# Optimization experiments

Measured on AMD Instinct MI355X. Metric: run time of the kernel, lower is better.

Reference implementation:

```python
import jax, jax.numpy as jnp
import numpy as np
from jax import lax
from jax.scipy.special import logsumexp

XY, Z, V, WS = 16, 8, 10000, 2
S = XY * XY * Z            # 2048 states
EMB, TOK, HID = 256, 100, 256
B, T, L = 8, 16, 12
EPS = 1e-5


def residual(x, w1, b1, w2, b2, g, beta):
    # ResidualLayer: relu(lin1) -> relu(lin2) -> LayerNorm(x2 + x1)
    x1 = jax.nn.relu(x @ w1.T + b1)
    x2 = jax.nn.relu(x1 @ w2.T + b2)
    h = x2 + x1
    mu = h.mean(-1, keepdims=True)
    var = ((h - mu) ** 2).mean(-1, keepdims=True)
    return (h - mu) * lax.rsqrt(var + EPS) * g + beta


def win_logmean(m, axis, ws):
    win = 2 * ws + 1
    pads = [(0, 0)] * m.ndim
    pads[axis] = (ws, ws)
    p = jnp.pad(m, pads, mode='edge')
    d = m.shape[axis]
    acc = lax.dynamic_slice_in_dim(p, 0, d, axis)
    for k in range(1, win):
        acc = jnp.logaddexp(acc, lax.dynamic_slice_in_dim(p, k, d, axis))
    return acc - jnp.log(jnp.float32(win))


def setup_inputs() -> dict:
    key = jax.random.key(0)
    it = iter(jax.random.split(key, 64))

    def rn(shape, scale=0.05):
        return jax.random.normal(next(it), shape, jnp.float32) * scale

    inp = {}
    inp['state_emb'] = jax.random.normal(next(it), (S, EMB), jnp.float32)
    inp['tok_emb'] = jax.random.normal(next(it), (V, TOK), jnp.float32)

    def res(pfx, din, dout):
        inp[pfx + '_w1'] = rn((dout, din))
        inp[pfx + '_b1'] = jnp.zeros((dout,), jnp.float32)
        inp[pfx + '_w2'] = rn((dout, dout))
        inp[pfx + '_b2'] = jnp.zeros((dout,), jnp.float32)
        inp[pfx + '_g'] = jnp.ones((dout,), jnp.float32)
        inp[pfx + '_beta'] = jnp.zeros((dout,), jnp.float32)

    res('start', EMB, HID)
    inp['start_wo'] = rn((1, HID))
    inp['start_bo'] = jnp.zeros((1,), jnp.float32)
    res('tin', EMB, HID)
    res('tout', EMB, HID)
    res('emit', EMB, TOK)
    inp['stories'] = jax.random.randint(next(it), (B, T, L), 0, V + 1)  # id V = pad
    inp['story_length'] = T
    return inp


def reference(state_emb, tok_emb,
              start_w1, start_b1, start_w2, start_b2, start_g, start_beta, start_wo, start_bo,
              tin_w1, tin_b1, tin_w2, tin_b2, tin_g, tin_beta,
              tout_w1, tout_b1, tout_w2, tout_b2, tout_g, tout_beta,
              emit_w1, emit_b1, emit_w2, emit_b2, emit_g, emit_beta,
              stories, story_length):
    # prior_log_p: [S]
    h0 = residual(state_emb, start_w1, start_b1, start_w2, start_b2, start_g, start_beta)
    priors = jax.nn.log_softmax((h0 @ start_wo.T + start_bo)[:, 0], axis=-1)

    # transition_log_p: sparse-neighbor masked [S,S] log-softmax
    h_in = residual(state_emb, tin_w1, tin_b1, tin_w2, tin_b2, tin_g, tin_beta)
    h_out = residual(state_emb, tout_w1, tout_b1, tout_w2, tout_b2, tout_g, tout_beta)
    trans = h_in @ h_out.T
    idx = jnp.arange(S)
    offs = jnp.array([0, 1, -1, XY, -XY, XY * XY, 2 * XY * XY])
    neigh = idx[:, None] + offs[None, :]                        # [S,7]
    allowed = (neigh[:, :, None] == idx[None, None, :]).any(1)  # allowed[j,i]
    trans = jax.nn.log_softmax(jnp.where(allowed, trans, -jnp.inf), axis=-1)

    # emission matrix with windowed log-mean pooling over x,y
    h_emit = residual(state_emb, emit_w1, emit_b1, emit_w2, emit_b2, emit_g, emit_beta)
    em = jax.nn.log_softmax(h_emit @ tok_emb.T, axis=1)         # [S,V]
    em = em.reshape(Z, XY, XY, V)
    em = win_logmean(em, 2, WS)   # dim -2
    em = win_logmean(em, 1, WS)   # dim -3
    em = em.reshape(S, V)
    em_pad = jnp.concatenate([em, jnp.zeros((S, 1), em.dtype)], axis=1)  # pad token
    emis = em_pad.T[stories].sum(2)                             # [B,T,S]

    # HMM forward recursion in log domain
    score0 = emis[:, 0] + priors[None, :]

    def step(score, em_t):
        new = em_t + logsumexp(trans[None, :, :] + score[:, None, :], axis=-1)
        return new, new

    _, rest = lax.scan(step, score0, jnp.moveaxis(emis[:, 1:story_length], 1, 0))
    return jnp.concatenate([score0[None], rest], axis=0)        # [T,B,S]
```

## Files before the change

kernel.cpp:

```cpp
#include <hip/hip_runtime.h>
#include <hip/hip_bf16.h>
#include <math.h>


typedef __bf16 bf16_t;
typedef __bf16 bf16x8 __attribute__((ext_vector_type(8)));
typedef float  floatx4 __attribute__((ext_vector_type(4)));
typedef short  short8  __attribute__((ext_vector_type(8)));

#define S_TOT 2048
#define NT_LSE 157
#define LSE_LD 160


struct CJob { const float* src; void* dst; int srows, scols, drows, dcols, tobf; };
struct CJobs { CJob j[12]; };

__global__ void conv_k(CJobs jobs) {
    CJob job = jobs.j[blockIdx.y];
    int total = job.drows * job.dcols;
    for (int idx = blockIdx.x * 256 + threadIdx.x; idx < total; idx += gridDim.x * 256) {
        int r = idx / job.dcols;
        int c = idx - r * job.dcols;
        float v = (r < job.srows && c < job.scols) ? job.src[(size_t)r * job.scols + c] : 0.f;
        if (job.tobf) ((bf16_t*)job.dst)[idx] = (bf16_t)v;
        else          ((float*)job.dst)[idx]  = v;
    }
}

struct GJob {
    const bf16_t* A; int lda;
    const bf16_t* Bt; int ldb;
    int N, K;
    float* C; int ldc;
    const float* bias;
    const float* addm; int ldadd;
    bf16_t* Cbf; int ldcb;
    float* Pmax; float* Psum;
};
struct GJobs { GJob j[4]; };

#define BM 64
#define BN 64
#define LDT 72

template<int EPI>
__global__ __launch_bounds__(256) void gemm_k(GJobs jobs) {
    GJob jb = jobs.j[blockIdx.z];
    const int m0 = blockIdx.x * BM;
    const int n0 = blockIdx.y * BN;
    if (n0 >= jb.N) return;

    __shared__ alignas(16) bf16_t As[BM * LDT];
    __shared__ alignas(16) bf16_t Bs[BN * LDT];
    const int tid  = threadIdx.x;
    const int lane = tid & 63, wave = tid >> 6;
    const int wm = (wave & 1) * 32, wn = (wave >> 1) * 32;
    const int sr = tid >> 2, scc = (tid & 3) * 16;
    const int qm = lane & 15, qk = (lane >> 4) * 8;

    floatx4 acc[2][2];
    floatx4 zf = {0.f, 0.f, 0.f, 0.f};
#pragma unroll
    for (int i = 0; i < 2; i++)
#pragma unroll
        for (int j = 0; j < 2; j++) acc[i][j] = zf;

    for (int k0 = 0; k0 < jb.K; k0 += 64) {
        const bf16_t* Ar = jb.A + (size_t)(m0 + sr) * jb.lda + k0 + scc;
        const bf16_t* Br = jb.Bt + (size_t)(n0 + sr) * jb.ldb + k0 + scc;
        *(short8*)&As[sr * LDT + scc]     = *(const short8*)&Ar[0];
        *(short8*)&As[sr * LDT + scc + 8] = *(const short8*)&Ar[8];
        *(short8*)&Bs[sr * LDT + scc]     = *(const short8*)&Br[0];
        *(short8*)&Bs[sr * LDT + scc + 8] = *(const short8*)&Br[8];
        __syncthreads();
#pragma unroll
        for (int kk = 0; kk < 2; kk++) {
            int qo = kk * 32 + qk;
            bf16x8 a[2], b[2];
            a[0] = *(const bf16x8*)&As[(wm + qm) * LDT + qo];
            a[1] = *(const bf16x8*)&As[(wm + 16 + qm) * LDT + qo];
            b[0] = *(const bf16x8*)&Bs[(wn + qm) * LDT + qo];
            b[1] = *(const bf16x8*)&Bs[(wn + 16 + qm) * LDT + qo];
#pragma unroll
            for (int mi = 0; mi < 2; mi++)
#pragma unroll
                for (int ni = 0; ni < 2; ni++)
                    acc[mi][ni] = __builtin_amdgcn_mfma_f32_16x16x32_bf16(a[mi], b[ni], acc[mi][ni], 0, 0, 0);
        }
        __syncthreads();
    }

    const int cl = lane & 15, rq = (lane >> 4) * 4;

    if constexpr (EPI == 3) {
        __shared__ float Cs[BM][BN + 1];
#pragma unroll
        for (int mi = 0; mi < 2; mi++)
#pragma unroll
            for (int ni = 0; ni < 2; ni++)
#pragma unroll
                for (int r = 0; r < 4; r++) {
                    int lm = wm + mi * 16 + rq + r;
                    int ln2 = wn + ni * 16 + cl;
                    Cs[lm][ln2] = (n0 + ln2 < jb.N) ? acc[mi][ni][r] : -INFINITY;
                }
        __syncthreads();
        int trow = tid >> 2, part = tid & 3;
        float m = -INFINITY;
#pragma unroll
        for (int c = 0; c < 16; c++) m = fmaxf(m, Cs[trow][part * 16 + c]);
        m = fmaxf(m, __shfl_xor(m, 1));
        m = fmaxf(m, __shfl_xor(m, 2));
        float ss = 0.f;
#pragma unroll
        for (int c = 0; c < 16; c++) ss += __expf(Cs[trow][part * 16 + c] - m);
        ss += __shfl_xor(ss, 1);
        ss += __shfl_xor(ss, 2);
        if (part == 0) {
            jb.Pmax[(size_t)(m0 + trow) * LSE_LD + blockIdx.y] = m;
            jb.Psum[(size_t)(m0 + trow) * LSE_LD + blockIdx.y] = ss;
        }
    } else {
#pragma unroll
        for (int mi = 0; mi < 2; mi++)
#pragma unroll
            for (int ni = 0; ni < 2; ni++)
#pragma unroll
                for (int r = 0; r < 4; r++) {
                    int gm = m0 + wm + mi * 16 + rq + r;
                    int gn = n0 + wn + ni * 16 + cl;
                    if (gn < jb.N) {
                        float v = acc[mi][ni][r];
                        if constexpr (EPI == 0) {
                            jb.C[(size_t)gm * jb.ldc + gn] = v;
                        } else if constexpr (EPI == 1) {
                            v = fmaxf(v + jb.bias[gn], 0.f);
                            jb.C[(size_t)gm * jb.ldc + gn] = v;
                            jb.Cbf[(size_t)gm * jb.ldcb + gn] = (bf16_t)v;
                        } else {
                            v = fmaxf(v + jb.bias[gn], 0.f) + jb.addm[(size_t)gm * jb.ldadd + gn];
                            jb.C[(size_t)gm * jb.ldc + gn] = v;
                        }
                    }
                }
    }
}

struct LJob {
    const float* h; int ld, dout;
    const float* g; const float* beta;
    float* of32; int ldo;
    bf16_t* obf; int ldob; int padN;
    const float* wo; const float* bo; float* praw;
};
struct LJobs { LJob j[4]; };

__global__ __launch_bounds__(256) void ln_k(LJobs jobs) {
    LJob jb = jobs.j[blockIdx.y];
    __shared__ float red[256];
    int row = blockIdx.x, t = threadIdx.x;
    float hv = (t < jb.dout) ? jb.h[(size_t)row * jb.ld + t] : 0.f;
    red[t] = hv;
    __syncthreads();
#pragma unroll
    for (int s = 128; s > 0; s >>= 1) { if (t < s) red[t] += red[t + s]; __syncthreads(); }
    float mu = red[0] / jb.dout;
    __syncthreads();
    float d = (t < jb.dout) ? (hv - mu) : 0.f;
    red[t] = d * d;
    __syncthreads();
#pragma unroll
    for (int s = 128; s > 0; s >>= 1) { if (t < s) red[t] += red[t + s]; __syncthreads(); }
    float var = red[0] / jb.dout;
    float rstd = rsqrtf(var + 1e-5f);
    float y = 0.f;
    if (t < jb.dout) {
        y = d * rstd * jb.g[t] + jb.beta[t];
        if (jb.of32) jb.of32[(size_t)row * jb.ldo + t] = y;
        if (jb.obf)  jb.obf[(size_t)row * jb.ldob + t] = (bf16_t)y;
    } else if (jb.obf && t < jb.padN) {
        jb.obf[(size_t)row * jb.ldob + t] = (bf16_t)0.f;
    }
    if (jb.wo) {
        __syncthreads();
        red[t] = (t < jb.dout) ? y * jb.wo[t] : 0.f;
        __syncthreads();
#pragma unroll
        for (int s = 128; s > 0; s >>= 1) { if (t < s) red[t] += red[t + s]; __syncthreads(); }
        if (t == 0) jb.praw[row] = red[0] + jb.bo[0];
    }
}

__global__ __launch_bounds__(256) void trans_k(const float* __restrict__ hin,
                                               const float* __restrict__ hout,
                                               float* __restrict__ tr,
                                               const float* __restrict__ praw,
                                               float* __restrict__ plse)
{
    __shared__ float red[256];
    if (blockIdx.x == 512) {
        int t = threadIdx.x;
        float v[8];
        float m = -INFINITY;
#pragma unroll
        for (int i = 0; i < 8; i++) { v[i] = praw[t * 8 + i]; m = fmaxf(m, v[i]); }
        red[t] = m;
        __syncthreads();
#pragma unroll
        for (int s = 128; s > 0; s >>= 1) { if (t < s) red[t] = fmaxf(red[t], red[t + s]); __syncthreads(); }
        float M = red[0];
        __syncthreads();
        float ss = 0.f;
#pragma unroll
        for (int i = 0; i < 8; i++) ss += __expf(v[i] - M);
        red[t] = ss;
        __syncthreads();
#pragma unroll
        for (int s = 128; s > 0; s >>= 1) { if (t < s) red[t] += red[t + s]; __syncthreads(); }
        if (t == 0) plse[0] = M + __logf(red[0]);
        return;
    }
    const int OFFS[7] = {0, 1, -1, 16, -16, 256, 512};
    int j = blockIdx.x * 4 + (threadIdx.x >> 6);
    int lane = threadIdx.x & 63;
    float4 a = ((const float4*)(hin + (size_t)j * 256))[lane];
    float d[7];
#pragma unroll
    for (int k = 0; k < 7; k++) {
        int i = j + OFFS[k];
        float pdot = 0.f;
        if ((unsigned)i < 2048u) {
            float4 b = ((const float4*)(hout + (size_t)i * 256))[lane];
            pdot = a.x * b.x + a.y * b.y + a.z * b.z + a.w * b.w;
        }
#pragma unroll
        for (int o = 32; o > 0; o >>= 1) pdot += __shfl_down(pdot, o);
        d[k] = pdot;
    }
    if (lane == 0) {
        float m = -INFINITY;
#pragma unroll
        for (int k = 0; k < 7; k++) { int i = j + OFFS[k]; if ((unsigned)i < 2048u) m = fmaxf(m, d[k]); }
        float ss = 0.f;
#pragma unroll
        for (int k = 0; k < 7; k++) { int i = j + OFFS[k]; if ((unsigned)i < 2048u) ss += __expf(d[k] - m); }
        float l = __logf(ss);
#pragma unroll
        for (int k = 0; k < 7; k++) {
            int i = j + OFFS[k];
            tr[(size_t)j * 8 + k] = ((unsigned)i < 2048u) ? (d[k] - m - l) : -INFINITY;
        }
        tr[(size_t)j * 8 + 7] = -INFINITY;
    }
}

__global__ __launch_bounds__(256) void lse_fin_k(const float* __restrict__ Pmax,
                                                 const float* __restrict__ Psum,
                                                 float* __restrict__ lse)
{
    int s = (blockIdx.x * 256 + threadIdx.x) >> 6;
    int lane = threadIdx.x & 63;
    const float* pm = Pmax + (size_t)s * LSE_LD;
    const float* ps = Psum + (size_t)s * LSE_LD;
    float pv[3], sv[3];
    float m = -INFINITY;
#pragma unroll
    for (int i = 0; i < 3; i++) {
        int nb = i * 64 + lane;
        bool ok = nb < NT_LSE;
        pv[i] = ok ? pm[nb] : -INFINITY;
        sv[i] = ok ? ps[nb] : 0.f;
        m = fmaxf(m, pv[i]);
    }
#pragma unroll
    for (int o = 1; o < 64; o <<= 1) m = fmaxf(m, __shfl_xor(m, o));
    float ss = 0.f;
#pragma unroll
    for (int i = 0; i < 3; i++) ss += sv[i] * __expf(pv[i] - m);
#pragma unroll
    for (int o = 1; o < 64; o <<= 1) ss += __shfl_xor(ss, o);
    if (lane == 0) lse[s] = m + __logf(ss);
}

#define ELDT 136
__global__ __launch_bounds__(256) void empool_k(
    const float* __restrict__ tok_emb, const int* __restrict__ stories,
    const bf16_t* __restrict__ hemit, const float* __restrict__ lse,
    float* __restrict__ emis)
{
    __shared__ alignas(16) bf16_t As[16 * ELDT];
    __shared__ float Cs[16][260];
    __shared__ float sm2[256];
    __shared__ int stok[12];
    const int bt = blockIdx.x, z = blockIdx.y, t = threadIdx.x;
    if (t < 12) stok[t] = stories[bt * 12 + t];
    __syncthreads();
    {
        int row = t >> 4, c0 = (t & 15) * 8;
        int tok = (row < 12) ? stok[row] : 10000;
        const float* src = tok_emb + (size_t)tok * 100;
#pragma unroll
        for (int c = 0; c < 8; c++) {
            int cc = c0 + c;
            float v = (tok < 10000 && cc < 100) ? src[cc] : 0.f;
            As[row * ELDT + cc] = (bf16_t)v;
        }
    }
    __syncthreads();

    const int lane = t & 63, wave = t >> 6;
    const int qm = lane & 15, q = lane >> 4;
    floatx4 acc[4];
    floatx4 zf = {0.f, 0.f, 0.f, 0.f};
#pragma unroll
    for (int j = 0; j < 4; j++) acc[j] = zf;

#pragma unroll
    for (int kk = 0; kk < 4; kk++) {
        bf16x8 a = *(const bf16x8*)&As[qm * ELDT + kk * 32 + q * 8];
#pragma unroll
        for (int j = 0; j < 4; j++) {
            int nrow = z * 256 + (wave * 4 + j) * 16 + qm;
            bf16x8 b = *(const bf16x8*)&hemit[(size_t)nrow * 128 + kk * 32 + q * 8];
            acc[j] = __builtin_amdgcn_mfma_f32_16x16x32_bf16(a, b, acc[j], 0, 0, 0);
        }
    }
    {
        const int cl = lane & 15, rq = (lane >> 4) * 4;
#pragma unroll
        for (int j = 0; j < 4; j++) {
            int n = (wave * 4 + j) * 16 + cl;
            float ls = lse[z * 256 + n];
#pragma unroll
            for (int r = 0; r < 4; r++)
                Cs[rq + r][n] = acc[j][r] - ls;
        }
    }
    __syncthreads();

    const int a = t >> 4, b = t & 15;
    float accum = 0.f;
    for (int l = 0; l < 12; l++) {
        float m = -INFINITY;
#pragma unroll
        for (int d = -2; d <= 2; d++) {
            int bb = b + d; bb = bb < 0 ? 0 : (bb > 15 ? 15 : bb);
            m = fmaxf(m, Cs[l][a * 16 + bb]);
        }
        float ss = 0.f;
#pragma unroll
        for (int d = -2; d <= 2; d++) {
            int bb = b + d; bb = bb < 0 ? 0 : (bb > 15 ? 15 : bb);
            ss += __expf(Cs[l][a * 16 + bb] - m);
        }
        sm2[t] = m + __logf(ss);
        __syncthreads();
        float m2 = -INFINITY;
#pragma unroll
        for (int d = -2; d <= 2; d++) {
            int aa = a + d; aa = aa < 0 ? 0 : (aa > 15 ? 15 : aa);
            m2 = fmaxf(m2, sm2[aa * 16 + b]);
        }
        float s2 = 0.f;
#pragma unroll
        for (int d = -2; d <= 2; d++) {
            int aa = a + d; aa = aa < 0 ? 0 : (aa > 15 ? 15 : aa);
            s2 += __expf(sm2[aa * 16 + b] - m2);
        }
        if (stok[l] < 10000) accum += m2 + __logf(s2) - 3.2188758248682006f;
        __syncthreads();
    }
    emis[(size_t)bt * S_TOT + (size_t)z * 256 + t] = accum;
}

__global__ __launch_bounds__(1024) void fwd_k(const float* __restrict__ emm,
                                              const float* __restrict__ praw,
                                              const float* __restrict__ plse,
                                              const float* __restrict__ tr,
                                              float* __restrict__ out)
{
    const int OFFS[7] = {0, 1, -1, 16, -16, 256, 512};
    __shared__ float sc[2][S_TOT];
    int b = blockIdx.x, t = threadIdx.x;
    float pl = plse[0];
    const float* eb = emm + (size_t)b * 16 * S_TOT;

    float e[2][16];
#pragma unroll
    for (int i = 0; i < 2; i++) {
        int j = i * 1024 + t;
#pragma unroll
        for (int tt = 0; tt < 16; tt++) e[i][tt] = eb[tt * S_TOT + j];
    }
    float trj[2][7];
#pragma unroll
    for (int i = 0; i < 2; i++) {
        int j = i * 1024 + t;
        float4 lo = ((const float4*)(tr + (size_t)j * 8))[0];
        float4 hi = ((const float4*)(tr + (size_t)j * 8))[1];
        trj[i][0] = lo.x; trj[i][1] = lo.y; trj[i][2] = lo.z; trj[i][3] = lo.w;
        trj[i][4] = hi.x; trj[i][5] = hi.y; trj[i][6] = hi.z;
    }
#pragma unroll
    for (int i = 0; i < 2; i++) {
        int j = i * 1024 + t;
        float v = e[i][0] + praw[j] - pl;
        sc[0][j] = v;
        out[(size_t)b * S_TOT + j] = v;
    }
    __syncthreads();
#pragma unroll
    for (int tt = 1; tt < 16; tt++) {
        int cur = tt & 1, prv = cur ^ 1;
#pragma unroll
        for (int i = 0; i < 2; i++) {
            int j = i * 1024 + t;
            float x[7];
            float m = -INFINITY;
#pragma unroll
            for (int k = 0; k < 7; k++) {
                int ii = j + OFFS[k];
                ii = ii < 0 ? 0 : (ii > 2047 ? 2047 : ii);
                x[k] = trj[i][k] + sc[prv][ii];
                m = fmaxf(m, x[k]);
            }
            float ss = 0.f;
#pragma unroll
            for (int k = 0; k < 7; k++) ss += __expf(x[k] - m);
            float v = e[i][tt] + m + __logf(ss);
            sc[cur][j] = v;
            out[(size_t)tt * (8 * S_TOT) + (size_t)b * S_TOT + j] = v;
        }
        __syncthreads();
    }
}

extern "C" void kernel_launch(void* const* d_in, const int* in_sizes, int n_in,
                              void* d_out, int out_size, void* d_ws, size_t ws_size,
                              hipStream_t stream)
{
    (void)in_sizes; (void)n_in; (void)out_size; (void)ws_size;
    const float* state_emb  = (const float*)d_in[0];
    const float* tok_emb    = (const float*)d_in[1];
    const float* start_w1   = (const float*)d_in[2];
    const float* start_b1   = (const float*)d_in[3];
    const float* start_w2   = (const float*)d_in[4];
    const float* start_b2   = (const float*)d_in[5];
    const float* start_g    = (const float*)d_in[6];
    const float* start_beta = (const float*)d_in[7];
    const float* start_wo   = (const float*)d_in[8];
    const float* start_bo   = (const float*)d_in[9];
    const float* tin_w1     = (const float*)d_in[10];
    const float* tin_b1     = (const float*)d_in[11];
    const float* tin_w2     = (const float*)d_in[12];
    const float* tin_b2     = (const float*)d_in[13];
    const float* tin_g      = (const float*)d_in[14];
    const float* tin_beta   = (const float*)d_in[15];
    const float* tout_w1    = (const float*)d_in[16];
    const float* tout_b1    = (const float*)d_in[17];
    const float* tout_w2    = (const float*)d_in[18];
    const float* tout_b2    = (const float*)d_in[19];
    const float* tout_g     = (const float*)d_in[20];
    const float* tout_beta  = (const float*)d_in[21];
    const float* emit_w1    = (const float*)d_in[22];
    const float* emit_b1    = (const float*)d_in[23];
    const float* emit_w2    = (const float*)d_in[24];
    const float* emit_b2    = (const float*)d_in[25];
    const float* emit_g     = (const float*)d_in[26];
    const float* emit_beta  = (const float*)d_in[27];
    const int*   stories    = (const int*)d_in[28];
    float* out = (float*)d_out;

    char* base = (char*)d_ws;
    size_t off = 0;
    auto carve = [&](size_t bytes) -> char* {
        char* r = base + off;
        off = (off + bytes + 255) & ~(size_t)255;
        return r;
    };

    bf16_t* se_bf   = (bf16_t*)carve((size_t)2048 * 256 * 2);
    bf16_t* tok_bf  = (bf16_t*)carve((size_t)10048 * 128 * 2);
    bf16_t* w_s1    = (bf16_t*)carve((size_t)256 * 256 * 2);
    bf16_t* w_s2    = (bf16_t*)carve((size_t)256 * 256 * 2);
    bf16_t* w_i1    = (bf16_t*)carve((size_t)256 * 256 * 2);
    bf16_t* w_i2    = (bf16_t*)carve((size_t)256 * 256 * 2);
    bf16_t* w_o1    = (bf16_t*)carve((size_t)256 * 256 * 2);
    bf16_t* w_o2    = (bf16_t*)carve((size_t)256 * 256 * 2);
    bf16_t* w_e1    = (bf16_t*)carve((size_t)128 * 256 * 2);
    bf16_t* w_e2    = (bf16_t*)carve((size_t)128 * 128 * 2);
    float*  eb1     = (float*)carve(128 * 4);
    float*  eb2     = (float*)carve(128 * 4);
    bf16_t* hemit   = (bf16_t*)carve((size_t)2048 * 128 * 2);
    float*  hin     = (float*)carve((size_t)2048 * 256 * 4);
    float*  hout    = (float*)carve((size_t)2048 * 256 * 4);
    float*  praw    = (float*)carve((size_t)2048 * 4);
    float*  plse    = (float*)carve(256);
    float*  trans   = (float*)carve((size_t)2048 * 8 * 4);
    float*  pmax    = (float*)carve((size_t)2048 * LSE_LD * 4);
    float*  psum    = (float*)carve((size_t)2048 * LSE_LD * 4);
    float*  lse     = (float*)carve((size_t)2048 * 4);
    float*  emis    = (float*)carve((size_t)128 * 2048 * 4);

    size_t ovl = off;
    auto carveA = [&](size_t bytes) -> char* {
        char* r = base + ovl;
        ovl = (ovl + bytes + 255) & ~(size_t)255;
        return r;
    };
    float*  x1f_s  = (float*)carveA((size_t)2048 * 256 * 4);
    float*  x1f_i  = (float*)carveA((size_t)2048 * 256 * 4);
    float*  x1f_o  = (float*)carveA((size_t)2048 * 256 * 4);
    float*  x1f_e  = (float*)carveA((size_t)2048 * 128 * 4);
    bf16_t* x1b_s  = (bf16_t*)carveA((size_t)2048 * 256 * 2);
    bf16_t* x1b_i  = (bf16_t*)carveA((size_t)2048 * 256 * 2);
    bf16_t* x1b_o  = (bf16_t*)carveA((size_t)2048 * 256 * 2);
    bf16_t* x1b_e  = (bf16_t*)carveA((size_t)2048 * 128 * 2);
    float*  htmp_s = (float*)carveA((size_t)2048 * 256 * 4);
    float*  htmp_i = (float*)carveA((size_t)2048 * 256 * 4);
    float*  htmp_o = (float*)carveA((size_t)2048 * 256 * 4);
    float*  htmp_e = (float*)carveA((size_t)2048 * 128 * 4);

    CJobs cj;
    cj.j[0]  = {state_emb, se_bf, 2048, 256, 2048, 256, 1};
    cj.j[1]  = {tok_emb,   tok_bf, 10000, 100, 10048, 128, 1};
    cj.j[2]  = {start_w1,  w_s1, 256, 256, 256, 256, 1};
    cj.j[3]  = {start_w2,  w_s2, 256, 256, 256, 256, 1};
    cj.j[4]  = {tin_w1,    w_i1, 256, 256, 256, 256, 1};
    cj.j[5]  = {tin_w2,    w_i2, 256, 256, 256, 256, 1};
    cj.j[6]  = {tout_w1,   w_o1, 256, 256, 256, 256, 1};
    cj.j[7]  = {tout_w2,   w_o2, 256, 256, 256, 256, 1};
    cj.j[8]  = {emit_w1,   w_e1, 100, 256, 128, 256, 1};
    cj.j[9]  = {emit_w2,   w_e2, 100, 100, 128, 128, 1};
    cj.j[10] = {emit_b1,   eb1, 1, 100, 1, 128, 0};
    cj.j[11] = {emit_b2,   eb2, 1, 100, 1, 128, 0};
    conv_k<<<dim3(160, 12), 256, 0, stream>>>(cj);

    GJobs g1;
    g1.j[0] = {se_bf, 256, w_s1, 256, 256, 256, x1f_s, 256, start_b1, nullptr, 0, x1b_s, 256, nullptr, nullptr};
    g1.j[1] = {se_bf, 256, w_i1, 256, 256, 256, x1f_i, 256, tin_b1,   nullptr, 0, x1b_i, 256, nullptr, nullptr};
    g1.j[2] = {se_bf, 256, w_o1, 256, 256, 256, x1f_o, 256, tout_b1,  nullptr, 0, x1b_o, 256, nullptr, nullptr};
    g1.j[3] = {se_bf, 256, w_e1, 256, 128, 256, x1f_e, 128, eb1,      nullptr, 0, x1b_e, 128, nullptr, nullptr};
    gemm_k<1><<<dim3(32, 4, 4), 256, 0, stream>>>(g1);

    GJobs g2;
    g2.j[0] = {x1b_s, 256, w_s2, 256, 256, 256, htmp_s, 256, start_b2, x1f_s, 256, nullptr, 0, nullptr, nullptr};
    g2.j[1] = {x1b_i, 256, w_i2, 256, 256, 256, htmp_i, 256, tin_b2,   x1f_i, 256, nullptr, 0, nullptr, nullptr};
    g2.j[2] = {x1b_o, 256, w_o2, 256, 256, 256, htmp_o, 256, tout_b2,  x1f_o, 256, nullptr, 0, nullptr, nullptr};
    g2.j[3] = {x1b_e, 128, w_e2, 128, 128, 128, htmp_e, 128, eb2,      x1f_e, 128, nullptr, 0, nullptr, nullptr};
    gemm_k<2><<<dim3(32, 4, 4), 256, 0, stream>>>(g2);

    LJobs lj;
    lj.j[0] = {htmp_s, 256, 256, start_g, start_beta, nullptr, 0, nullptr, 0, 0, start_wo, start_bo, praw};
    lj.j[1] = {htmp_i, 256, 256, tin_g,   tin_beta,   hin, 256, nullptr, 0, 0, nullptr, nullptr, nullptr};
    lj.j[2] = {htmp_o, 256, 256, tout_g,  tout_beta,  hout, 256, nullptr, 0, 0, nullptr, nullptr, nullptr};
    lj.j[3] = {htmp_e, 128, 100, emit_g,  emit_beta,  nullptr, 0, hemit, 128, 128, nullptr, nullptr, nullptr};
    ln_k<<<dim3(2048, 4), 256, 0, stream>>>(lj);

    trans_k<<<513, 256, 0, stream>>>(hin, hout, trans, praw, plse);

    GJobs g3;
    g3.j[0] = {hemit, 128, tok_bf, 128, 10000, 128, nullptr, 0, nullptr, nullptr, 0, nullptr, 0, pmax, psum};
    gemm_k<3><<<dim3(32, NT_LSE, 1), 256, 0, stream>>>(g3);
    lse_fin_k<<<512, 256, 0, stream>>>(pmax, psum, lse);

    empool_k<<<dim3(128, 8), 256, 0, stream>>>(tok_emb, stories, hemit, lse, emis);

    fwd_k<<<8, 1024, 0, stream>>>(emis, praw, plse, trans, out);
}
```

Before: 221.8 us.

## Fuse fp32-to-bf16 conversion into GEMM loads and enlarge the vocab LSE GEMM tile

Drops the separate conversion kernel: the GEMMs now read fp32 weights, embeddings and tok_emb directly and convert to bf16 while staging into shared memory, with K and row padding handled by predicates. The vocab logsumexp GEMM becomes a dedicated kernel with 128x128 tiles and 4x4 MFMA per wave. It reduces partial max and sum within the block, halving the partial count that lse_fin_k combines. This removes one launch and the bf16 staging buffers' traffic, at the cost of extra conversion work in every GEMM tile load and higher register pressure in the larger tile.

```diff
diff --git a/kernel.cpp b/kernel.cpp
--- a/kernel.cpp
+++ b/kernel.cpp
@@ -9,34 +9,19 @@
 typedef short  short8  __attribute__((ext_vector_type(8)));
 
 #define S_TOT 2048
-#define NT_LSE 157
-#define LSE_LD 160
-
-
-struct CJob { const float* src; void* dst; int srows, scols, drows, dcols, tobf; };
-struct CJobs { CJob j[12]; };
-
-__global__ void conv_k(CJobs jobs) {
-    CJob job = jobs.j[blockIdx.y];
-    int total = job.drows * job.dcols;
-    for (int idx = blockIdx.x * 256 + threadIdx.x; idx < total; idx += gridDim.x * 256) {
-        int r = idx / job.dcols;
-        int c = idx - r * job.dcols;
-        float v = (r < job.srows && c < job.scols) ? job.src[(size_t)r * job.scols + c] : 0.f;
-        if (job.tobf) ((bf16_t*)job.dst)[idx] = (bf16_t)v;
-        else          ((float*)job.dst)[idx]  = v;
-    }
-}
+#define NT2 79
+#define LSE_LD 80
 
 struct GJob {
-    const bf16_t* A; int lda;
-    const bf16_t* Bt; int ldb;
-    int N, K;
+    const float*  Af;
+    const bf16_t* Ab;
+    int lda;
+    const float* B; int ldb;
+    int N, Nrows, K, Kvalid;
     float* C; int ldc;
-    const float* bias;
+    const float* bias; int nbias;
     const float* addm; int ldadd;
     bf16_t* Cbf; int ldcb;
-    float* Pmax; float* Psum;
 };
 struct GJobs { GJob j[4]; };
 
@@ -44,7 +29,7 @@
 #define BN 64
 #define LDT 72
 
-template<int EPI>
+template<int EPI, int A32>
 __global__ __launch_bounds__(256) void gemm_k(GJobs jobs) {
     GJob jb = jobs.j[blockIdx.z];
     const int m0 = blockIdx.x * BM;
@@ -66,13 +51,39 @@
 #pragma unroll
         for (int j = 0; j < 2; j++) acc[i][j] = zf;
 
+    const bool brv = (n0 + sr) < jb.Nrows;
+
     for (int k0 = 0; k0 < jb.K; k0 += 64) {
-        const bf16_t* Ar = jb.A + (size_t)(m0 + sr) * jb.lda + k0 + scc;
-        const bf16_t* Br = jb.Bt + (size_t)(n0 + sr) * jb.ldb + k0 + scc;
-        *(short8*)&As[sr * LDT + scc]     = *(const short8*)&Ar[0];
-        *(short8*)&As[sr * LDT + scc + 8] = *(const short8*)&Ar[8];
-        *(short8*)&Bs[sr * LDT + scc]     = *(const short8*)&Br[0];
-        *(short8*)&Bs[sr * LDT + scc + 8] = *(const short8*)&Br[8];
+        if constexpr (A32) {
+            const float* Ar = jb.Af + (size_t)(m0 + sr) * jb.lda + k0 + scc;
+            alignas(16) bf16_t ta[16];
+#pragma unroll
+            for (int i = 0; i < 4; i++) {
+                float4 f = ((const float4*)Ar)[i];
+                ta[i * 4 + 0] = (bf16_t)f.x; ta[i * 4 + 1] = (bf16_t)f.y;
+                ta[i * 4 + 2] = (bf16_t)f.z; ta[i * 4 + 3] = (bf16_t)f.w;
+            }
+            *(short8*)&As[sr * LDT + scc]     = *(short8*)&ta[0];
+            *(short8*)&As[sr * LDT + scc + 8] = *(short8*)&ta[8];
+        } else {
+            const bf16_t* Ar = jb.Ab + (size_t)(m0 + sr) * jb.lda + k0 + scc;
+            *(short8*)&As[sr * LDT + scc]     = *(const short8*)&Ar[0];
+            *(short8*)&As[sr * LDT + scc + 8] = *(const short8*)&Ar[8];
+        }
+        {
+            const float* Br = jb.B + (size_t)(n0 + sr) * jb.ldb + k0 + scc;
+            alignas(16) bf16_t tb[16];
+#pragma unroll
+            for (int i = 0; i < 4; i++) {
+                int c4 = k0 + scc + i * 4;
+                float4 f = {0.f, 0.f, 0.f, 0.f};
+                if (brv && c4 < jb.Kvalid) f = *(const float4*)&Br[i * 4];
+                tb[i * 4 + 0] = (bf16_t)f.x; tb[i * 4 + 1] = (bf16_t)f.y;
+                tb[i * 4 + 2] = (bf16_t)f.z; tb[i * 4 + 3] = (bf16_t)f.w;
+            }
+            *(short8*)&Bs[sr * LDT + scc]     = *(short8*)&tb[0];
+            *(short8*)&Bs[sr * LDT + scc + 8] = *(short8*)&tb[8];
+        }
         __syncthreads();
 #pragma unroll
         for (int kk = 0; kk < 2; kk++) {
@@ -92,59 +103,25 @@
     }
 
     const int cl = lane & 15, rq = (lane >> 4) * 4;
-
-    if constexpr (EPI == 3) {
-        __shared__ float Cs[BM][BN + 1];
-#pragma unroll
-        for (int mi = 0; mi < 2; mi++)
-#pragma unroll
-            for (int ni = 0; ni < 2; ni++)
-#pragma unroll
-                for (int r = 0; r < 4; r++) {
-                    int lm = wm + mi * 16 + rq + r;
-                    int ln2 = wn + ni * 16 + cl;
-                    Cs[lm][ln2] = (n0 + ln2 < jb.N) ? acc[mi][ni][r] : -INFINITY;
-                }
-        __syncthreads();
-        int trow = tid >> 2, part = tid & 3;
-        float m = -INFINITY;
-#pragma unroll
-        for (int c = 0; c < 16; c++) m = fmaxf(m, Cs[trow][part * 16 + c]);
-        m = fmaxf(m, __shfl_xor(m, 1));
-        m = fmaxf(m, __shfl_xor(m, 2));
-        float ss = 0.f;
-#pragma unroll
-        for (int c = 0; c < 16; c++) ss += __expf(Cs[trow][part * 16 + c] - m);
-        ss += __shfl_xor(ss, 1);
-        ss += __shfl_xor(ss, 2);
-        if (part == 0) {
-            jb.Pmax[(size_t)(m0 + trow) * LSE_LD + blockIdx.y] = m;
-            jb.Psum[(size_t)(m0 + trow) * LSE_LD + blockIdx.y] = ss;
-        }
-    } else {
-#pragma unroll
-        for (int mi = 0; mi < 2; mi++)
-#pragma unroll
-            for (int ni = 0; ni < 2; ni++)
-#pragma unroll
-                for (int r = 0; r < 4; r++) {
-                    int gm = m0 + wm + mi * 16 + rq + r;
-                    int gn = n0 + wn + ni * 16 + cl;
-                    if (gn < jb.N) {
-                        float v = acc[mi][ni][r];
-                        if constexpr (EPI == 0) {
-                            jb.C[(size_t)gm * jb.ldc + gn] = v;
-                        } else if constexpr (EPI == 1) {
-                            v = fmaxf(v + jb.bias[gn], 0.f);
-                            jb.C[(size_t)gm * jb.ldc + gn] = v;
-                            jb.Cbf[(size_t)gm * jb.ldcb + gn] = (bf16_t)v;
-                        } else {
-                            v = fmaxf(v + jb.bias[gn], 0.f) + jb.addm[(size_t)gm * jb.ldadd + gn];
-                            jb.C[(size_t)gm * jb.ldc + gn] = v;
-                        }
+#pragma unroll
+    for (int mi = 0; mi < 2; mi++)
+#pragma unroll
+        for (int ni = 0; ni < 2; ni++)
+#pragma unroll
+            for (int r = 0; r < 4; r++) {
+                int gm = m0 + wm + mi * 16 + rq + r;
+                int gn = n0 + wn + ni * 16 + cl;
+                if (gn < jb.N) {
+                    float bv = (gn < jb.nbias) ? jb.bias[gn] : 0.f;
+                    float v = fmaxf(acc[mi][ni][r] + bv, 0.f);
+                    if constexpr (EPI == 1) {
+                        jb.C[(size_t)gm * jb.ldc + gn] = v;
+                        jb.Cbf[(size_t)gm * jb.ldcb + gn] = (bf16_t)v;
+                    } else {
+                        jb.C[(size_t)gm * jb.ldc + gn] = v + jb.addm[(size_t)gm * jb.ldadd + gn];
                     }
                 }
-    }
+            }
 }
 
 struct LJob {
@@ -255,6 +232,114 @@
     }
 }
 
+#define LDT2 72
+__global__ __launch_bounds__(256) void lse_gemm_k(
+    const bf16_t* __restrict__ hemit, const float* __restrict__ tok_emb,
+    float* __restrict__ Pmax, float* __restrict__ Psum)
+{
+    __shared__ alignas(16) bf16_t As[128 * LDT2];
+    __shared__ alignas(16) bf16_t Bs[128 * LDT2];
+    __shared__ float pmS[2][128];
+    __shared__ float psS[2][128];
+    const int mb = blockIdx.x * 128;
+    const int n0 = blockIdx.y * 128;
+    const int tid  = threadIdx.x;
+    const int lane = tid & 63, wave = tid >> 6;
+    const int wm = (wave & 1) * 64, wn = (wave >> 1) * 64;
+    const int sr2 = tid >> 1, scc2 = (tid & 1) * 32;
+    const int qm = lane & 15, qk = (lane >> 4) * 8;
+
+    floatx4 acc[4][4];
+    floatx4 zf = {0.f, 0.f, 0.f, 0.f};
+#pragma unroll
+    for (int i = 0; i < 4; i++)
+#pragma unroll
+        for (int j = 0; j < 4; j++) acc[i][j] = zf;
+
+    const bool brv = (n0 + sr2) < 10000;
+    const float* Brow = tok_emb + (size_t)(n0 + sr2) * 100;
+    const bf16_t* Arow = hemit + (size_t)(mb + sr2) * 128;
+
+#pragma unroll
+    for (int k0 = 0; k0 < 128; k0 += 64) {
+#pragma unroll
+        for (int i = 0; i < 4; i++)
+            *(short8*)&As[sr2 * LDT2 + scc2 + i * 8] = *(const short8*)&Arow[k0 + scc2 + i * 8];
+        {
+            alignas(16) bf16_t tb[32];
+#pragma unroll
+            for (int i = 0; i < 8; i++) {
+                int c4 = k0 + scc2 + i * 4;
+                float4 f = {0.f, 0.f, 0.f, 0.f};
+                if (brv && c4 < 100) f = *(const float4*)&Brow[c4];
+                tb[i * 4 + 0] = (bf16_t)f.x; tb[i * 4 + 1] = (bf16_t)f.y;
+                tb[i * 4 + 2] = (bf16_t)f.z; tb[i * 4 + 3] = (bf16_t)f.w;
+            }
+#pragma unroll
+            for (int i = 0; i < 4; i++)
+                *(short8*)&Bs[sr2 * LDT2 + scc2 + i * 8] = *(short8*)&tb[i * 8];
+        }
+        __syncthreads();
+#pragma unroll
+        for (int kk = 0; kk < 2; kk++) {
+            int qo = kk * 32 + qk;
+            bf16x8 a[4], b[4];
+#pragma unroll
+            for (int mi = 0; mi < 4; mi++) a[mi] = *(const bf16x8*)&As[(wm + mi * 16 + qm) * LDT2 + qo];
+#pragma unroll
+            for (int ni = 0; ni < 4; ni++) b[ni] = *(const bf16x8*)&Bs[(wn + ni * 16 + qm) * LDT2 + qo];
+#pragma unroll
+            for (int mi = 0; mi < 4; mi++)
+#pragma unroll
+                for (int ni = 0; ni < 4; ni++)
+                    acc[mi][ni] = __builtin_amdgcn_mfma_f32_16x16x32_bf16(a[mi], b[ni], acc[mi][ni], 0, 0, 0);
+        }
+        __syncthreads();
+    }
+
+    const int cl = lane & 15, rq = (lane >> 4) * 4;
+    const int half = wn >> 6;
+#pragma unroll
+    for (int mi = 0; mi < 4; mi++) {
+#pragma unroll
+        for (int r = 0; r < 4; r++) {
+            float mm = -INFINITY;
+#pragma unroll
+            for (int ni = 0; ni < 4; ni++) {
+                int gcol = n0 + wn + ni * 16 + cl;
+                if (gcol < 10000) mm = fmaxf(mm, acc[mi][ni][r]);
+            }
+            mm = fmaxf(mm, __shfl_xor(mm, 1));
+            mm = fmaxf(mm, __shfl_xor(mm, 2));
+            mm = fmaxf(mm, __shfl_xor(mm, 4));
+            mm = fmaxf(mm, __shfl_xor(mm, 8));
+            float ss = 0.f;
+#pragma unroll
+            for (int ni = 0; ni < 4; ni++) {
+                int gcol = n0 + wn + ni * 16 + cl;
+                if (gcol < 10000) ss += __expf(acc[mi][ni][r] - mm);
+            }
+            ss += __shfl_xor(ss, 1);
+            ss += __shfl_xor(ss, 2);
+            ss += __shfl_xor(ss, 4);
+            ss += __shfl_xor(ss, 8);
+            if (cl == 0) {
+                int row = wm + mi * 16 + rq + r;
+                pmS[half][row] = mm;
+                psS[half][row] = ss;
+            }
+        }
+    }
+    __syncthreads();
+    if (tid < 128) {
+        float ma = pmS[0][tid], mb2 = pmS[1][tid];
+        float M = fmaxf(ma, mb2);
+        float S = psS[0][tid] * __expf(ma - M) + psS[1][tid] * __expf(mb2 - M);
+        Pmax[(size_t)(mb + tid) * LSE_LD + blockIdx.y] = M;
+        Psum[(size_t)(mb + tid) * LSE_LD + blockIdx.y] = S;
+    }
+}
+
 __global__ __launch_bounds__(256) void lse_fin_k(const float* __restrict__ Pmax,
                                                  const float* __restrict__ Psum,
                                                  float* __restrict__ lse)
@@ -263,12 +348,12 @@
     int lane = threadIdx.x & 63;
     const float* pm = Pmax + (size_t)s * LSE_LD;
     const float* ps = Psum + (size_t)s * LSE_LD;
-    float pv[3], sv[3];
+    float pv[2], sv[2];
     float m = -INFINITY;
 #pragma unroll
-    for (int i = 0; i < 3; i++) {
+    for (int i = 0; i < 2; i++) {
         int nb = i * 64 + lane;
-        bool ok = nb < NT_LSE;
+        bool ok = nb < NT2;
         pv[i] = ok ? pm[nb] : -INFINITY;
         sv[i] = ok ? ps[nb] : 0.f;
         m = fmaxf(m, pv[i]);
@@ -277,7 +362,7 @@
     for (int o = 1; o < 64; o <<= 1) m = fmaxf(m, __shfl_xor(m, o));
     float ss = 0.f;
 #pragma unroll
-    for (int i = 0; i < 3; i++) ss += sv[i] * __expf(pv[i] - m);
+    for (int i = 0; i < 2; i++) if (sv[i] > 0.f) ss += sv[i] * __expf(pv[i] - m);
 #pragma unroll
     for (int o = 1; o < 64; o <<= 1) ss += __shfl_xor(ss, o);
     if (lane == 0) lse[s] = m + __logf(ss);
@@ -480,76 +565,43 @@
         return r;
     };
 
-    bf16_t* se_bf   = (bf16_t*)carve((size_t)2048 * 256 * 2);
-    bf16_t* tok_bf  = (bf16_t*)carve((size_t)10048 * 128 * 2);
-    bf16_t* w_s1    = (bf16_t*)carve((size_t)256 * 256 * 2);
-    bf16_t* w_s2    = (bf16_t*)carve((size_t)256 * 256 * 2);
-    bf16_t* w_i1    = (bf16_t*)carve((size_t)256 * 256 * 2);
-    bf16_t* w_i2    = (bf16_t*)carve((size_t)256 * 256 * 2);
-    bf16_t* w_o1    = (bf16_t*)carve((size_t)256 * 256 * 2);
-    bf16_t* w_o2    = (bf16_t*)carve((size_t)256 * 256 * 2);
-    bf16_t* w_e1    = (bf16_t*)carve((size_t)128 * 256 * 2);
-    bf16_t* w_e2    = (bf16_t*)carve((size_t)128 * 128 * 2);
-    float*  eb1     = (float*)carve(128 * 4);
-    float*  eb2     = (float*)carve(128 * 4);
-    bf16_t* hemit   = (bf16_t*)carve((size_t)2048 * 128 * 2);
-    float*  hin     = (float*)carve((size_t)2048 * 256 * 4);
-    float*  hout    = (float*)carve((size_t)2048 * 256 * 4);
-    float*  praw    = (float*)carve((size_t)2048 * 4);
-    float*  plse    = (float*)carve(256);
-    float*  trans   = (float*)carve((size_t)2048 * 8 * 4);
-    float*  pmax    = (float*)carve((size_t)2048 * LSE_LD * 4);
-    float*  psum    = (float*)carve((size_t)2048 * LSE_LD * 4);
-    float*  lse     = (float*)carve((size_t)2048 * 4);
-    float*  emis    = (float*)carve((size_t)128 * 2048 * 4);
-
-    size_t ovl = off;
-    auto carveA = [&](size_t bytes) -> char* {
-        char* r = base + ovl;
-        ovl = (ovl + bytes + 255) & ~(size_t)255;
-        return r;
-    };
-    float*  x1f_s  = (float*)carveA((size_t)2048 * 256 * 4);
-    float*  x1f_i  = (float*)carveA((size_t)2048 * 256 * 4);
-    float*  x1f_o  = (float*)carveA((size_t)2048 * 256 * 4);
-    float*  x1f_e  = (float*)carveA((size_t)2048 * 128 * 4);
-    bf16_t* x1b_s  = (bf16_t*)carveA((size_t)2048 * 256 * 2);
-    bf16_t* x1b_i  = (bf16_t*)carveA((size_t)2048 * 256 * 2);
-    bf16_t* x1b_o  = (bf16_t*)carveA((size_t)2048 * 256 * 2);
-    bf16_t* x1b_e  = (bf16_t*)carveA((size_t)2048 * 128 * 2);
-    float*  htmp_s = (float*)carveA((size_t)2048 * 256 * 4);
-    float*  htmp_i = (float*)carveA((size_t)2048 * 256 * 4);
-    float*  htmp_o = (float*)carveA((size_t)2048 * 256 * 4);
-    float*  htmp_e = (float*)carveA((size_t)2048 * 128 * 4);
-
-    CJobs cj;
-    cj.j[0]  = {state_emb, se_bf, 2048, 256, 2048, 256, 1};
-    cj.j[1]  = {tok_emb,   tok_bf, 10000, 100, 10048, 128, 1};
-    cj.j[2]  = {start_w1,  w_s1, 256, 256, 256, 256, 1};
-    cj.j[3]  = {start_w2,  w_s2, 256, 256, 256, 256, 1};
-    cj.j[4]  = {tin_w1,    w_i1, 256, 256, 256, 256, 1};
-    cj.j[5]  = {tin_w2,    w_i2, 256, 256, 256, 256, 1};
-    cj.j[6]  = {tout_w1,   w_o1, 256, 256, 256, 256, 1};
-    cj.j[7]  = {tout_w2,   w_o2, 256, 256, 256, 256, 1};
-    cj.j[8]  = {emit_w1,   w_e1, 100, 256, 128, 256, 1};
-    cj.j[9]  = {emit_w2,   w_e2, 100, 100, 128, 128, 1};
-    cj.j[10] = {emit_b1,   eb1, 1, 100, 1, 128, 0};
-    cj.j[11] = {emit_b2,   eb2, 1, 100, 1, 128, 0};
-    conv_k<<<dim3(160, 12), 256, 0, stream>>>(cj);
+    bf16_t* hemit = (bf16_t*)carve((size_t)2048 * 128 * 2);
+    float*  hin   = (float*)carve((size_t)2048 * 256 * 4);
+    float*  hout  = (float*)carve((size_t)2048 * 256 * 4);
+    float*  praw  = (float*)carve((size_t)2048 * 4);
+    float*  plse  = (float*)carve(256);
+    float*  trans = (float*)carve((size_t)2048 * 8 * 4);
+    float*  pmax  = (float*)carve((size_t)2048 * LSE_LD * 4);
+    float*  psum  = (float*)carve((size_t)2048 * LSE_LD * 4);
+    float*  lse   = (float*)carve((size_t)2048 * 4);
+    float*  emis  = (float*)carve((size_t)128 * 2048 * 4);
+
+    float*  x1f_s  = (float*)carve((size_t)2048 * 256 * 4);
+    float*  x1f_i  = (float*)carve((size_t)2048 * 256 * 4);
+    float*  x1f_o  = (float*)carve((size_t)2048 * 256 * 4);
+    float*  x1f_e  = (float*)carve((size_t)2048 * 128 * 4);
+    bf16_t* x1b_s  = (bf16_t*)carve((size_t)2048 * 256 * 2);
+    bf16_t* x1b_i  = (bf16_t*)carve((size_t)2048 * 256 * 2);
+    bf16_t* x1b_o  = (bf16_t*)carve((size_t)2048 * 256 * 2);
+    bf16_t* x1b_e  = (bf16_t*)carve((size_t)2048 * 128 * 2);
+    float*  htmp_s = (float*)carve((size_t)2048 * 256 * 4);
+    float*  htmp_i = (float*)carve((size_t)2048 * 256 * 4);
+    float*  htmp_o = (float*)carve((size_t)2048 * 256 * 4);
+    float*  htmp_e = (float*)carve((size_t)2048 * 128 * 4);
 
     GJobs g1;
-    g1.j[0] = {se_bf, 256, w_s1, 256, 256, 256, x1f_s, 256, start_b1, nullptr, 0, x1b_s, 256, nullptr, nullptr};
-    g1.j[1] = {se_bf, 256, w_i1, 256, 256, 256, x1f_i, 256, tin_b1,   nullptr, 0, x1b_i, 256, nullptr, nullptr};
-    g1.j[2] = {se_bf, 256, w_o1, 256, 256, 256, x1f_o, 256, tout_b1,  nullptr, 0, x1b_o, 256, nullptr, nullptr};
-    g1.j[3] = {se_bf, 256, w_e1, 256, 128, 256, x1f_e, 128, eb1,      nullptr, 0, x1b_e, 128, nullptr, nullptr};
-    gemm_k<1><<<dim3(32, 4, 4), 256, 0, stream>>>(g1);
+    g1.j[0] = {state_emb, nullptr, 256, start_w1, 256, 256, 256, 256, 256, x1f_s, 256, start_b1, 256, nullptr, 0, x1b_s, 256};
+    g1.j[1] = {state_emb, nullptr, 256, tin_w1,   256, 256, 256, 256, 256, x1f_i, 256, tin_b1,   256, nullptr, 0, x1b_i, 256};
+    g1.j[2] = {state_emb, nullptr, 256, tout_w1,  256, 256, 256, 256, 256, x1f_o, 256, tout_b1,  256, nullptr, 0, x1b_o, 256};
+    g1.j[3] = {state_emb, nullptr, 256, emit_w1,  256, 128, 100, 256, 256, x1f_e, 128, emit_b1,  100, nullptr, 0, x1b_e, 128};
+    gemm_k<1, 1><<<dim3(32, 4, 4), 256, 0, stream>>>(g1);
 
     GJobs g2;
-    g2.j[0] = {x1b_s, 256, w_s2, 256, 256, 256, htmp_s, 256, start_b2, x1f_s, 256, nullptr, 0, nullptr, nullptr};
-    g2.j[1] = {x1b_i, 256, w_i2, 256, 256, 256, htmp_i, 256, tin_b2,   x1f_i, 256, nullptr, 0, nullptr, nullptr};
-    g2.j[2] = {x1b_o, 256, w_o2, 256, 256, 256, htmp_o, 256, tout_b2,  x1f_o, 256, nullptr, 0, nullptr, nullptr};
-    g2.j[3] = {x1b_e, 128, w_e2, 128, 128, 128, htmp_e, 128, eb2,      x1f_e, 128, nullptr, 0, nullptr, nullptr};
-    gemm_k<2><<<dim3(32, 4, 4), 256, 0, stream>>>(g2);
+    g2.j[0] = {nullptr, x1b_s, 256, start_w2, 256, 256, 256, 256, 256, htmp_s, 256, start_b2, 256, x1f_s, 256, nullptr, 0};
+    g2.j[1] = {nullptr, x1b_i, 256, tin_w2,   256, 256, 256, 256, 256, htmp_i, 256, tin_b2,   256, x1f_i, 256, nullptr, 0};
+    g2.j[2] = {nullptr, x1b_o, 256, tout_w2,  256, 256, 256, 256, 256, htmp_o, 256, tout_b2,  256, x1f_o, 256, nullptr, 0};
+    g2.j[3] = {nullptr, x1b_e, 128, emit_w2,  100, 128, 100, 128, 100, htmp_e, 128, emit_b2,  100, x1f_e, 128, nullptr, 0};
+    gemm_k<2, 0><<<dim3(32, 4, 4), 256, 0, stream>>>(g2);
 
     LJobs lj;
     lj.j[0] = {htmp_s, 256, 256, start_g, start_beta, nullptr, 0, nullptr, 0, 0, start_wo, start_bo, praw};
@@ -560,9 +612,7 @@
 
     trans_k<<<513, 256, 0, stream>>>(hin, hout, trans, praw, plse);
 
-    GJobs g3;
-    g3.j[0] = {hemit, 128, tok_bf, 128, 10000, 128, nullptr, 0, nullptr, nullptr, 0, nullptr, 0, pmax, psum};
-    gemm_k<3><<<dim3(32, NT_LSE, 1), 256, 0, stream>>>(g3);
+    lse_gemm_k<<<dim3(16, NT2), 256, 0, stream>>>(hemit, tok_emb, pmax, psum);
     lse_fin_k<<<512, 256, 0, stream>>>(pmax, psum, lse);
 
     empool_k<<<dim3(128, 8), 256, 0, stream>>>(tok_emb, stories, hemit, lse, emis);
```

Measured after the change: 223.6 us. No clear change (+0.8%).
